# Kernel tuning notes

Hardware: AMD Instinct MI355X
Metric: run time of the kernel (lower is better)

## Reference

```python
import jax, jax.numpy as jnp
import numpy as np

B, N, NG = 32, 64, 100   # batch, atoms, gaussians in srdf
NB, NF, MAXZ = 128, 256, 20  # n_basis, n_factors, max atomic number
N_INTERACTIONS = 3


def setup_inputs() -> dict:
    key = jax.random.key(0)
    ks = jax.random.split(key, 12)
    r = np.sqrt(1.0 / np.sqrt(float(NB))).astype(np.float32)
    return {
        "Z": jax.random.randint(ks[0], (B, N), 0, MAXZ, dtype=jnp.int32),
        "C": jax.random.uniform(ks[1], (B, N, N, NG), dtype=jnp.float32),
        # learned parameters
        "W_emb": jax.random.normal(ks[2], (MAXZ, NB), dtype=jnp.float32) * r,
        "Wc": jax.random.normal(ks[3], (NG, NF), dtype=jnp.float32) * 0.1,
        "bc": jnp.zeros((NF,), dtype=jnp.float32),
        "Wi": jax.random.normal(ks[4], (NB, NF), dtype=jnp.float32) * 0.1,  # in2fac (shared across passes)
        "bi": jnp.zeros((NF,), dtype=jnp.float32),
        "Wf": jax.random.normal(ks[5], (NF, NB), dtype=jnp.float32) * 0.1,  # fac2out (shared)
        "W1": jax.random.normal(ks[6], (NB, NB // 2), dtype=jnp.float32) * 0.1,
        "b1": jnp.zeros((NB // 2,), dtype=jnp.float32),
        "W2": jax.random.normal(ks[7], (NB // 2, 1), dtype=jnp.float32) * 0.1,
        "b2": jnp.zeros((1,), dtype=jnp.float32),
    }


def reference(Z, C, W_emb, Wc, bc, Wi, bi, Wf, W1, b1, W2, b2):
    # pairwise mask: valid atom pairs (Z_i>0 and Z_j>0), diagonal removed
    pair = Z[:, :, None] * Z[:, None, :]                      # [B,N,N]
    offdiag = 1.0 - jnp.eye(N, dtype=jnp.float32)
    mask = (pair > 0).astype(jnp.float32) * offdiag           # [B,N,N]
    mask = mask[..., None]                                    # [B,N,N,1]

    # atom embedding via one-hot lookup == row gather
    X = W_emb[Z]                                              # [B,N,NB]
    # distance basis -> factor space
    fC = jnp.einsum('bijg,gf->bijf', C, Wc) + bc              # [B,N,N,NF]

    for _ in range(N_INTERACTIONS):
        fX = X @ Wi + bi                                      # [B,N,NF]
        fVj = fX[:, None, :, :] * fC                          # [B,N,N,NF]
        Vj = jnp.tanh(jnp.einsum('bijf,fo->bijo', fVj, Wf))   # [B,N,N,NB]
        V = jnp.sum(Vj * mask, axis=2)                        # masked sum over neighbors j
        X = X + V

    o1 = jnp.tanh(X @ W1 + b1)                                # [B,N,NB//2]
    yi = o1 @ W2 + b2                                         # [B,N,1]; std=1, mu=0 -> identity
    atom_mask = (Z > 0).astype(jnp.float32)[..., None]        # [B,N,1]
    y = jnp.sum(yi * atom_mask, axis=1)                       # [B,1] total energy
    return y
```

## Files before the change

### kernel.cpp

```cpp
#include <hip/hip_runtime.h>
#include <hip/hip_bf16.h>
#include <math.h>

#define BB   32
#define NN   64
#define NGG  100
#define NBB  128
#define NFF  256
#define NITER 3
#define KPAD 128

typedef _Float16 f16x8 __attribute__((ext_vector_type(8)));
typedef _Float16 f16x4 __attribute__((ext_vector_type(4)));
typedef float    f32x4 __attribute__((ext_vector_type(4)));

static __device__ __forceinline__ float fast_exp2(float x) {
    float r; asm("v_exp_f32 %0, %1" : "=v"(r) : "v"(x)); return r;
}
static __device__ __forceinline__ float fast_rcp(float x) {
    float r; asm("v_rcp_f32 %0, %1" : "=v"(r) : "v"(x)); return r;
}
static __device__ __forceinline__ float fast_tanh(float x) {
    float p = fast_exp2(x * 2.8853900817779268f);
    return 1.0f - 2.0f * fast_rcp(p + 1.0f);
}

#define EMB_N (BB * NN * NBB)
#define WCF_N (NFF * KPAD)
#define WFF_N (NBB * NFF)
__global__ void prep_kernel(const int* __restrict__ Z, const float* __restrict__ W_emb,
                            const float* __restrict__ Wc, const float* __restrict__ Wf,
                            float* __restrict__ X, _Float16* __restrict__ WcF,
                            _Float16* __restrict__ WfF) {
    int idx = blockIdx.x * 256 + threadIdx.x;
    if (idx < EMB_N) {
        int bn = idx >> 7, t = idx & 127;
        X[idx] = W_emb[Z[bn] * NBB + t];
        return;
    }
    idx -= EMB_N;
    if (idx < WCF_N) {
        int e = idx & 7, lane = (idx >> 3) & 63, ks = (idx >> 9) & 3, ct = (idx >> 11) & 3, w = idx >> 13;
        int l15 = lane & 15, kg = lane >> 4;
        int f = w * 64 + ct * 16 + l15;
        int k = ks * 32 + kg * 8 + e;
        WcF[idx] = (k < NGG) ? (_Float16)Wc[(size_t)k * NFF + f] : (_Float16)0.f;
        return;
    }
    idx -= WCF_N;
    if (idx < WFF_N) {
        int e = idx & 7, lane = (idx >> 3) & 63, ks = (idx >> 9) & 7, ct = (idx >> 12) & 1, w = idx >> 13;
        int l15 = lane & 15, kg = lane >> 4;
        int o = w * 32 + ct * 16 + l15;
        int k = ks * 32 + kg * 8 + e;
        WfF[idx] = (_Float16)Wf[(size_t)k * NBB + o];
    }
}
#define PREP_GRID ((EMB_N + WCF_N + WFF_N) / 256)

__global__ void transpose_pad_kernel(const float* __restrict__ src, _Float16* __restrict__ dst,
                                     int K, int Kpad, int NC) {
    int idx = blockIdx.x * 256 + threadIdx.x;
    if (idx >= NC * Kpad) return;
    int c = idx / Kpad, k = idx - c * Kpad;
    dst[idx] = (k < K) ? (_Float16)src[(size_t)k * NC + c] : (_Float16)0.f;
}

__global__ void fx_kernel(const float* __restrict__ X, const float* __restrict__ Wi,
                          const float* __restrict__ bi, const int* __restrict__ Z,
                          _Float16* __restrict__ fXF) {
    __shared__ float Xs[NBB];
    int bn = blockIdx.x, t = threadIdx.x;
    if (t < NBB) Xs[t] = X[bn * NBB + t];
    __syncthreads();
    float acc = bi[t];
    for (int k = 0; k < NBB; ++k) acc += Xs[k] * Wi[k * NFF + t];
    int b = bn >> 6, jr = bn & 63;
    int jt = jr >> 4, l15 = jr & 15;
    int ks = t >> 5, kg2 = (t >> 3) & 3, e = t & 7;
    size_t off = ((size_t)(b * 32 + jt * 8 + ks) * 64 + (kg2 * 16 + l15)) * 8 + e;
    fXF[off] = (Z[bn] > 0) ? (_Float16)acc : (_Float16)0.f;
}

static __device__ __forceinline__ void stage_C(const float* Crow_base, _Float16* Cs, int t) {
    const int r = t >> 2, q = t & 3;
    const float* Crow = Crow_base + (size_t)r * NGG;
    const int sw = (r & 7) << 3;
    #pragma unroll
    for (int m = 0; m < 8; ++m) {
        const int k = q * 32 + m * 4;
        f16x4 h = {0.f, 0.f, 0.f, 0.f};
        if (k < NGG) {
            float4 v = *(const float4*)(Crow + k);
            h[0] = (_Float16)v.x; h[1] = (_Float16)v.y;
            h[2] = (_Float16)v.z; h[3] = (_Float16)v.w;
        }
        *(f16x4*)&Cs[r * KPAD + (k ^ sw)] = h;
    }
}

__global__ __launch_bounds__(256, 3) void fc_kernel(
    const int* __restrict__ Z, const float* __restrict__ C,
    const _Float16* __restrict__ WcF, const float* __restrict__ bc,
    _Float16* __restrict__ fCF)
{
    __shared__ __align__(16) _Float16 Cs[NN * KPAD];
    const int bi_ = blockIdx.x;
    const int b = bi_ >> 6, i = bi_ & 63;
    if (Z[b * NN + i] == 0) return;

    const int t = threadIdx.x;
    const int wave = t >> 6, lane = t & 63;
    const int l15 = lane & 15, kg = lane >> 4;

    stage_C(C + (size_t)bi_ * NN * NGG, Cs, t);

    f16x8 aw[4][4];
    float4 bcq[4];
    #pragma unroll
    for (int ct = 0; ct < 4; ++ct) {
        #pragma unroll
        for (int ks = 0; ks < 4; ++ks)
            aw[ct][ks] = *(const f16x8*)&WcF[(size_t)(((wave * 4 + ct) * 4 + ks) * 64 + lane) * 8];
        bcq[ct] = *(const float4*)&bc[wave * 64 + ct * 16 + kg * 4];
    }
    __syncthreads();

    #pragma unroll
    for (int jt = 0; jt < 4; ++jt) {
        const int j = jt * 16 + l15;
        const int sw = (l15 & 7) << 3;
        f16x8 bfr[4];
        #pragma unroll
        for (int ks = 0; ks < 4; ++ks)
            bfr[ks] = *(const f16x8*)&Cs[j * KPAD + ((ks * 32 + kg * 8) ^ sw)];
        #pragma unroll
        for (int ct = 0; ct < 4; ++ct) {
            f32x4 acc = {bcq[ct].x, bcq[ct].y, bcq[ct].z, bcq[ct].w};
            #pragma unroll
            for (int ks = 0; ks < 4; ++ks)
                acc = __builtin_amdgcn_mfma_f32_16x16x32_f16(aw[ct][ks], bfr[ks], acc, 0, 0, 0);
            const int u = ct * 16 + kg * 4;
            const int ksf = wave * 2 + (u >> 5);
            const int kgf = (u >> 3) & 3;
            const int e0 = u & 4;
            f16x4 o;
            o[0] = (_Float16)acc[0]; o[1] = (_Float16)acc[1];
            o[2] = (_Float16)acc[2]; o[3] = (_Float16)acc[3];
            size_t off = ((size_t)(bi_ * 32 + jt * 8 + ksf) * 64 + (kgf * 16 + l15)) * 8 + e0;
            *(f16x4*)&fCF[off] = o;
        }
    }
}

__global__ __launch_bounds__(256) void interact_lite(
    const int* __restrict__ Z, const _Float16* __restrict__ fCF,
    const _Float16* __restrict__ WfF, const _Float16* __restrict__ fXF,
    float* __restrict__ X)
{
    const int bi_ = blockIdx.x;
    const int b = bi_ >> 6, i = bi_ & 63;
    if (Z[b * NN + i] == 0) return;

    const int t = threadIdx.x;
    const int wave = t >> 6, lane = t & 63;
    const int kg = lane >> 4;

    f16x8 bwf[2][8];
    #pragma unroll
    for (int ct = 0; ct < 2; ++ct)
        #pragma unroll
        for (int ks = 0; ks < 8; ++ks)
            bwf[ct][ks] = *(const f16x8*)&WfF[(size_t)(((wave * 2 + ct) * 8 + ks) * 64 + lane) * 8];

    const size_t cbase = (size_t)bi_ * 32;
    const size_t xbase = (size_t)b * 32;

    f32x4 a[4][2];
    #pragma unroll
    for (int jt = 0; jt < 4; ++jt) {
        a[jt][0] = (f32x4){0.f, 0.f, 0.f, 0.f};
        a[jt][1] = (f32x4){0.f, 0.f, 0.f, 0.f};
    }

    #pragma unroll
    for (int ks = 0; ks < 8; ++ks) {
        #pragma unroll
        for (int jt = 0; jt < 4; ++jt) {
            f16x8 fc = *(const f16x8*)&fCF[((cbase + jt * 8 + ks) * 64 + lane) * 8];
            f16x8 fx = *(const f16x8*)&fXF[((xbase + jt * 8 + ks) * 64 + lane) * 8];
            f16x8 av = fc * fx;
            a[jt][0] = __builtin_amdgcn_mfma_f32_16x16x32_f16(av, bwf[0][ks], a[jt][0], 0, 0, 0);
            a[jt][1] = __builtin_amdgcn_mfma_f32_16x16x32_f16(av, bwf[1][ks], a[jt][1], 0, 0, 0);
        }
    }

    float vsum0 = 0.f, vsum1 = 0.f;
    #pragma unroll
    for (int jt = 0; jt < 4; ++jt) {
        #pragma unroll
        for (int reg = 0; reg < 4; ++reg) {
            int j2 = jt * 16 + kg * 4 + reg;
            if (j2 != i) {
                vsum0 += fast_tanh(a[jt][0][reg]);
                vsum1 += fast_tanh(a[jt][1][reg]);
            }
        }
    }
    vsum0 += __shfl_xor(vsum0, 16); vsum0 += __shfl_xor(vsum0, 32);
    vsum1 += __shfl_xor(vsum1, 16); vsum1 += __shfl_xor(vsum1, 32);
    if (lane < 16) {
        float* Xp = X + (size_t)bi_ * NBB + wave * 32 + lane;
        Xp[0]  += vsum0;
        Xp[16] += vsum1;
    }
}

__global__ __launch_bounds__(256, 3) void interact_fused(
    const int* __restrict__ Z, const float* __restrict__ C,
    const _Float16* __restrict__ WcT, const float* __restrict__ bc,
    const _Float16* __restrict__ WfT, const _Float16* __restrict__ fXF,
    float* __restrict__ X)
{
    __shared__ __align__(16) _Float16 Cs[NN * KPAD];
    __shared__ __align__(16) _Float16 fVs[NN * NFF];

    const int bi_ = blockIdx.x;
    const int b = bi_ >> 6, i = bi_ & 63;
    if (Z[b * NN + i] == 0) return;

    const int t = threadIdx.x;
    const int wave = t >> 6, lane = t & 63;
    const int l15 = lane & 15, kg = lane >> 4;

    stage_C(C + (size_t)bi_ * NN * NGG, Cs, t);

    f16x8 aw[4][4];
    float4 bcq[4];
    #pragma unroll
    for (int ct = 0; ct < 4; ++ct) {
        #pragma unroll
        for (int ks = 0; ks < 4; ++ks)
            aw[ct][ks] = *(const f16x8*)&WcT[(size_t)(wave * 64 + ct * 16 + l15) * KPAD + ks * 32 + kg * 8];
        bcq[ct] = *(const float4*)&bc[wave * 64 + ct * 16 + kg * 4];
    }
    __syncthreads();

    #pragma unroll
    for (int jt = 0; jt < 4; ++jt) {
        const int j = jt * 16 + l15;
        const int sw = (l15 & 7) << 3;
        f16x8 bfr[4];
        #pragma unroll
        for (int ks = 0; ks < 4; ++ks)
            bfr[ks] = *(const f16x8*)&Cs[j * KPAD + ((ks * 32 + kg * 8) ^ sw)];
        #pragma unroll
        for (int ct = 0; ct < 4; ++ct) {
            f32x4 acc = {bcq[ct].x, bcq[ct].y, bcq[ct].z, bcq[ct].w};
            #pragma unroll
            for (int ks = 0; ks < 4; ++ks)
                acc = __builtin_amdgcn_mfma_f32_16x16x32_f16(aw[ct][ks], bfr[ks], acc, 0, 0, 0);
            const int u = ct * 16 + kg * 4;
            const int ksf = wave * 2 + (u >> 5);
            const int kgf = (u >> 3) & 3;
            const int e0 = u & 4;
            f16x4 fx4 = *(const f16x4*)&fXF[((size_t)(b * 32 + jt * 8 + ksf) * 64 + (kgf * 16 + l15)) * 8 + e0];
            const int f0 = wave * 64 + u;
            f16x4 o;
            o[0] = (_Float16)(acc[0] * (float)fx4[0]);
            o[1] = (_Float16)(acc[1] * (float)fx4[1]);
            o[2] = (_Float16)(acc[2] * (float)fx4[2]);
            o[3] = (_Float16)(acc[3] * (float)fx4[3]);
            *(f16x4*)&fVs[j * NFF + (f0 ^ ((j & 7) << 3))] = o;
        }
    }
    __syncthreads();

    f16x8 bwf[2][8];
    #pragma unroll
    for (int ct = 0; ct < 2; ++ct)
        #pragma unroll
        for (int ks = 0; ks < 8; ++ks)
            bwf[ct][ks] = *(const f16x8*)&WfT[(size_t)(wave * 32 + ct * 16 + l15) * NFF + ks * 32 + kg * 8];

    float vsum0 = 0.f, vsum1 = 0.f;
    #pragma unroll
    for (int jt = 0; jt < 4; ++jt) {
        const int r = jt * 16 + l15;
        const int sw = (l15 & 7) << 3;
        f32x4 a0 = {0.f, 0.f, 0.f, 0.f}, a1 = {0.f, 0.f, 0.f, 0.f};
        #pragma unroll
        for (int ks = 0; ks < 8; ++ks) {
            f16x8 av = *(const f16x8*)&fVs[r * NFF + ((ks * 32 + kg * 8) ^ sw)];
            a0 = __builtin_amdgcn_mfma_f32_16x16x32_f16(av, bwf[0][ks], a0, 0, 0, 0);
            a1 = __builtin_amdgcn_mfma_f32_16x16x32_f16(av, bwf[1][ks], a1, 0, 0, 0);
        }
        #pragma unroll
        for (int reg = 0; reg < 4; ++reg) {
            int j2 = jt * 16 + kg * 4 + reg;
            if (j2 != i) {
                vsum0 += fast_tanh(a0[reg]);
                vsum1 += fast_tanh(a1[reg]);
            }
        }
    }
    vsum0 += __shfl_xor(vsum0, 16); vsum0 += __shfl_xor(vsum0, 32);
    vsum1 += __shfl_xor(vsum1, 16); vsum1 += __shfl_xor(vsum1, 32);
    if (lane < 16) {
        float* Xp = X + (size_t)bi_ * NBB + wave * 32 + lane;
        Xp[0]  += vsum0;
        Xp[16] += vsum1;
    }
}

__global__ void readoutA_kernel(const int* __restrict__ Z, const float* __restrict__ X,
                                const float* __restrict__ W1, const float* __restrict__ b1,
                                const float* __restrict__ W2, const float* __restrict__ b2,
                                float* __restrict__ yi_buf)
{
    __shared__ float Xs[NBB];
    int bn = blockIdx.x;
    int h = threadIdx.x;
    Xs[h] = X[(size_t)bn * NBB + h];
    Xs[h + 64] = X[(size_t)bn * NBB + h + 64];
    __syncthreads();

    float s = b1[h];
    for (int k = 0; k < NBB; ++k) s += Xs[k] * W1[k * 64 + h];
    float v = tanhf(s) * W2[h];
    #pragma unroll
    for (int off = 32; off > 0; off >>= 1) v += __shfl_down(v, off);
    if (h == 0) {
        int z = Z[bn];
        yi_buf[bn] = (z > 0) ? (v + b2[0]) : 0.f;
    }
}

__global__ void readoutB_kernel(const float* __restrict__ yi_buf, float* __restrict__ y)
{
    int b = blockIdx.x, i = threadIdx.x;
    float v = yi_buf[b * NN + i];
    #pragma unroll
    for (int off = 32; off > 0; off >>= 1) v += __shfl_down(v, off);
    if (i == 0) y[b] = v;
}

extern "C" void kernel_launch(void* const* d_in, const int* in_sizes, int n_in,
                              void* d_out, int out_size, void* d_ws, size_t ws_size,
                              hipStream_t stream) {
    (void)in_sizes; (void)n_in; (void)out_size;
    const int*   Z    = (const int*)d_in[0];
    const float* C    = (const float*)d_in[1];
    const float* Wemb = (const float*)d_in[2];
    const float* Wc   = (const float*)d_in[3];
    const float* bc   = (const float*)d_in[4];
    const float* Wi   = (const float*)d_in[5];
    const float* bi   = (const float*)d_in[6];
    const float* Wf   = (const float*)d_in[7];
    const float* W1   = (const float*)d_in[8];
    const float* b1   = (const float*)d_in[9];
    const float* W2   = (const float*)d_in[10];
    const float* b2   = (const float*)d_in[11];
    float* y = (float*)d_out;

    char* p = (char*)d_ws;
    float*    X   = (float*)p;      p += (size_t)BB * NN * NBB * 4;
    _Float16* fXF = (_Float16*)p;   p += (size_t)BB * NN * NFF * 2;
    _Float16* WcF = (_Float16*)p;   p += (size_t)NFF * KPAD * 2;
    _Float16* WfF = (_Float16*)p;   p += (size_t)NBB * NFF * 2;
    _Float16* WcT = (_Float16*)p;   p += (size_t)NFF * KPAD * 2;
    _Float16* WfT = (_Float16*)p;   p += (size_t)NBB * NFF * 2;
    float*    yi  = (float*)p;      p += (size_t)BB * NN * 4;
    size_t base = (size_t)(p - (char*)d_ws);
    size_t fcf_bytes = (size_t)BB * NN * NN * NFF * 2;
    bool split = (ws_size >= base + fcf_bytes);
    _Float16* fCF = (_Float16*)p;

    prep_kernel<<<PREP_GRID, 256, 0, stream>>>(Z, Wemb, Wc, Wf, X, WcF, WfF);

    if (split) {
        fc_kernel<<<BB * NN, 256, 0, stream>>>(Z, C, WcF, bc, fCF);
        for (int it = 0; it < NITER; ++it) {
            fx_kernel<<<BB * NN, NFF, 0, stream>>>(X, Wi, bi, Z, fXF);
            interact_lite<<<BB * NN, 256, 0, stream>>>(Z, fCF, WfF, fXF, X);
        }
    } else {
        transpose_pad_kernel<<<(NFF * KPAD) / 256, 256, 0, stream>>>(Wc, WcT, NGG, KPAD, NFF);
        transpose_pad_kernel<<<(NBB * NFF) / 256, 256, 0, stream>>>(Wf, WfT, NFF, NFF, NBB);
        for (int it = 0; it < NITER; ++it) {
            fx_kernel<<<BB * NN, NFF, 0, stream>>>(X, Wi, bi, Z, fXF);
            interact_fused<<<BB * NN, 256, 0, stream>>>(Z, C, WcT, bc, WfT, fXF, X);
        }
    }
    readoutA_kernel<<<BB * NN, 64, 0, stream>>>(Z, X, W1, b1, W2, b2, yi);
    readoutB_kernel<<<BB, NN, 0, stream>>>(yi, y);
}
```

Measured before the change: 154.3 us.

## Use MFMA for fX and readout GEMMs, fuse first fX into fC kernel

Replaces the scalar per-atom fx_kernel with an MFMA-based fxm kernel that computes a whole batch's 64x256 factor tile per block, using a pre-swizzled fp16 Wi. The first iteration's fX is merged into the fC kernel as extra blocks, removing one launch. The readout is also rewritten as a single MFMA kernel with in-block reduction, replacing two launches. This cuts launch count and the scalar FMA loops, at the cost of fp16 rounding of X and the weights in these GEMMs.

Result: faster. 124.9 us (-19.0%).

```diff
diff --git a/kernel.cpp b/kernel.cpp
--- a/kernel.cpp
+++ b/kernel.cpp
@@ -28,10 +28,16 @@
 #define EMB_N (BB * NN * NBB)
 #define WCF_N (NFF * KPAD)
 #define WFF_N (NBB * NFF)
+#define WIF_N (NBB * NFF)
+#define W1F_N (NBB * 64)
+#define PREP_TOTAL (EMB_N + WCF_N + WFF_N + WIF_N + W1F_N)
+#define PREP_GRID (PREP_TOTAL / 256)
 __global__ void prep_kernel(const int* __restrict__ Z, const float* __restrict__ W_emb,
                             const float* __restrict__ Wc, const float* __restrict__ Wf,
+                            const float* __restrict__ Wi, const float* __restrict__ W1,
                             float* __restrict__ X, _Float16* __restrict__ WcF,
-                            _Float16* __restrict__ WfF) {
+                            _Float16* __restrict__ WfF, _Float16* __restrict__ WiF,
+                            _Float16* __restrict__ W1F) {
     int idx = blockIdx.x * 256 + threadIdx.x;
     if (idx < EMB_N) {
         int bn = idx >> 7, t = idx & 127;
@@ -54,9 +60,26 @@
         int o = w * 32 + ct * 16 + l15;
         int k = ks * 32 + kg * 8 + e;
         WfF[idx] = (_Float16)Wf[(size_t)k * NBB + o];
-    }
-}
-#define PREP_GRID ((EMB_N + WCF_N + WFF_N) / 256)
+        return;
+    }
+    idx -= WFF_N;
+    if (idx < WIF_N) {
+        int e = idx & 7, lane = (idx >> 3) & 63, ks = (idx >> 9) & 3, ct16 = idx >> 11;
+        int l15 = lane & 15, kg = lane >> 4;
+        int f = ct16 * 16 + l15;
+        int k = ks * 32 + kg * 8 + e;
+        WiF[idx] = (_Float16)Wi[(size_t)k * NFF + f];
+        return;
+    }
+    idx -= WIF_N;
+    if (idx < W1F_N) {
+        int e = idx & 7, lane = (idx >> 3) & 63, ks = (idx >> 9) & 3, ct16 = idx >> 11;
+        int l15 = lane & 15, kg = lane >> 4;
+        int o = ct16 * 16 + l15;
+        int k = ks * 32 + kg * 8 + e;
+        W1F[idx] = (_Float16)W1[(size_t)k * 64 + o];
+    }
+}
 
 __global__ void transpose_pad_kernel(const float* __restrict__ src, _Float16* __restrict__ dst,
                                      int K, int Kpad, int NC) {
@@ -64,22 +87,6 @@
     if (idx >= NC * Kpad) return;
     int c = idx / Kpad, k = idx - c * Kpad;
     dst[idx] = (k < K) ? (_Float16)src[(size_t)k * NC + c] : (_Float16)0.f;
-}
-
-__global__ void fx_kernel(const float* __restrict__ X, const float* __restrict__ Wi,
-                          const float* __restrict__ bi, const int* __restrict__ Z,
-                          _Float16* __restrict__ fXF) {
-    __shared__ float Xs[NBB];
-    int bn = blockIdx.x, t = threadIdx.x;
-    if (t < NBB) Xs[t] = X[bn * NBB + t];
-    __syncthreads();
-    float acc = bi[t];
-    for (int k = 0; k < NBB; ++k) acc += Xs[k] * Wi[k * NFF + t];
-    int b = bn >> 6, jr = bn & 63;
-    int jt = jr >> 4, l15 = jr & 15;
-    int ks = t >> 5, kg2 = (t >> 3) & 3, e = t & 7;
-    size_t off = ((size_t)(b * 32 + jt * 8 + ks) * 64 + (kg2 * 16 + l15)) * 8 + e;
-    fXF[off] = (Z[bn] > 0) ? (_Float16)acc : (_Float16)0.f;
 }
 
 static __device__ __forceinline__ void stage_C(const float* Crow_base, _Float16* Cs, int t) {
@@ -98,18 +105,30 @@
         *(f16x4*)&Cs[r * KPAD + (k ^ sw)] = h;
     }
 }
-
-__global__ __launch_bounds__(256, 3) void fc_kernel(
+static __device__ __forceinline__ void stage_X(const float* Xrow_base, _Float16* Xs, int t) {
+    const int r = t >> 2, q = t & 3;
+    const float* Xrow = Xrow_base + (size_t)r * NBB;
+    const int sw = (r & 7) << 3;
+    #pragma unroll
+    for (int m = 0; m < 8; ++m) {
+        const int k = q * 32 + m * 4;
+        float4 v = *(const float4*)(Xrow + k);
+        f16x4 h;
+        h[0] = (_Float16)v.x; h[1] = (_Float16)v.y;
+        h[2] = (_Float16)v.z; h[3] = (_Float16)v.w;
+        *(f16x4*)&Xs[r * KPAD + (k ^ sw)] = h;
+    }
+}
+
+static __device__ __forceinline__ void fc_body(
+    int bi_, int t, _Float16* Cs,
     const int* __restrict__ Z, const float* __restrict__ C,
     const _Float16* __restrict__ WcF, const float* __restrict__ bc,
     _Float16* __restrict__ fCF)
 {
-    __shared__ __align__(16) _Float16 Cs[NN * KPAD];
-    const int bi_ = blockIdx.x;
     const int b = bi_ >> 6, i = bi_ & 63;
     if (Z[b * NN + i] == 0) return;
 
-    const int t = threadIdx.x;
     const int wave = t >> 6, lane = t & 63;
     const int l15 = lane & 15, kg = lane >> 4;
 
@@ -151,6 +170,81 @@
             *(f16x4*)&fCF[off] = o;
         }
     }
+}
+
+static __device__ __forceinline__ void fxm_body(
+    int b, int fq, int t, _Float16* Xs,
+    const float* __restrict__ X, const _Float16* __restrict__ WiF,
+    const float* __restrict__ bi, const int* __restrict__ Z,
+    _Float16* __restrict__ fXF)
+{
+    const int wave = t >> 6, lane = t & 63;
+    const int l15 = lane & 15, kg = lane >> 4;
+    const int ct16 = fq * 4 + wave;
+
+    stage_X(X + (size_t)b * NN * NBB, Xs, t);
+
+    f16x8 aw[4];
+    #pragma unroll
+    for (int ks = 0; ks < 4; ++ks)
+        aw[ks] = *(const f16x8*)&WiF[(size_t)((ct16 * 4 + ks) * 64 + lane) * 8];
+    float4 biq = *(const float4*)&bi[ct16 * 16 + kg * 4];
+    __syncthreads();
+
+    f32x4 acc[4];
+    #pragma unroll
+    for (int jt = 0; jt < 4; ++jt) acc[jt] = (f32x4){biq.x, biq.y, biq.z, biq.w};
+
+    #pragma unroll
+    for (int ks = 0; ks < 4; ++ks) {
+        #pragma unroll
+        for (int jt = 0; jt < 4; ++jt) {
+            const int j = jt * 16 + l15;
+            const int sw = (l15 & 7) << 3;
+            f16x8 bfr = *(const f16x8*)&Xs[j * KPAD + ((ks * 32 + kg * 8) ^ sw)];
+            acc[jt] = __builtin_amdgcn_mfma_f32_16x16x32_f16(aw[ks], bfr, acc[jt], 0, 0, 0);
+        }
+    }
+
+    const int u_g = ct16 * 16 + kg * 4;
+    const int ks_t = u_g >> 5, kg_t = (u_g >> 3) & 3, e0 = u_g & 4;
+    #pragma unroll
+    for (int jt = 0; jt < 4; ++jt) {
+        const int j = jt * 16 + l15;
+        const int zj = Z[b * NN + j];
+        f16x4 o = {0.f, 0.f, 0.f, 0.f};
+        if (zj > 0) {
+            o[0] = (_Float16)acc[jt][0]; o[1] = (_Float16)acc[jt][1];
+            o[2] = (_Float16)acc[jt][2]; o[3] = (_Float16)acc[jt][3];
+        }
+        size_t off = ((size_t)(b * 32 + jt * 8 + ks_t) * 64 + (kg_t * 16 + l15)) * 8 + e0;
+        *(f16x4*)&fXF[off] = o;
+    }
+}
+
+#define FXM_GRID (BB * 4)
+
+__global__ __launch_bounds__(256) void fxm_kernel(
+    const float* __restrict__ X, const _Float16* __restrict__ WiF,
+    const float* __restrict__ bi, const int* __restrict__ Z,
+    _Float16* __restrict__ fXF)
+{
+    __shared__ __align__(16) _Float16 Xs[NN * KPAD];
+    fxm_body(blockIdx.x >> 2, blockIdx.x & 3, threadIdx.x, Xs, X, WiF, bi, Z, fXF);
+}
+
+__global__ __launch_bounds__(256, 3) void fcfx_kernel(
+    const int* __restrict__ Z, const float* __restrict__ C,
+    const _Float16* __restrict__ WcF, const float* __restrict__ bc,
+    _Float16* __restrict__ fCF,
+    const float* __restrict__ X, const _Float16* __restrict__ WiF,
+    const float* __restrict__ bi, _Float16* __restrict__ fXF)
+{
+    __shared__ __align__(16) _Float16 S[NN * KPAD];
+    if (blockIdx.x < FXM_GRID)
+        fxm_body(blockIdx.x >> 2, blockIdx.x & 3, threadIdx.x, S, X, WiF, bi, Z, fXF);
+    else
+        fc_body(blockIdx.x - FXM_GRID, threadIdx.x, S, Z, C, WcF, bc, fCF);
 }
 
 __global__ __launch_bounds__(256) void interact_lite(
@@ -313,36 +407,59 @@
     }
 }
 
-__global__ void readoutA_kernel(const int* __restrict__ Z, const float* __restrict__ X,
-                                const float* __restrict__ W1, const float* __restrict__ b1,
-                                const float* __restrict__ W2, const float* __restrict__ b2,
-                                float* __restrict__ yi_buf)
-{
-    __shared__ float Xs[NBB];
-    int bn = blockIdx.x;
-    int h = threadIdx.x;
-    Xs[h] = X[(size_t)bn * NBB + h];
-    Xs[h + 64] = X[(size_t)bn * NBB + h + 64];
+__global__ __launch_bounds__(256) void readout_kernel(
+    const int* __restrict__ Z, const float* __restrict__ X,
+    const _Float16* __restrict__ W1F, const float* __restrict__ b1,
+    const float* __restrict__ W2, const float* __restrict__ b2,
+    float* __restrict__ y)
+{
+    __shared__ __align__(16) _Float16 Xs[NN * KPAD];
+    __shared__ float part[4][NN];
+    const int b = blockIdx.x, t = threadIdx.x;
+    const int wave = t >> 6, lane = t & 63;
+    const int l15 = lane & 15, kg = lane >> 4;
+
+    stage_X(X + (size_t)b * NN * NBB, Xs, t);
+
+    f16x8 aw[4];
+    #pragma unroll
+    for (int ks = 0; ks < 4; ++ks)
+        aw[ks] = *(const f16x8*)&W1F[(size_t)((wave * 4 + ks) * 64 + lane) * 8];
+    float4 b1q = *(const float4*)&b1[wave * 16 + kg * 4];
+    float4 w2q = *(const float4*)&W2[wave * 16 + kg * 4];
     __syncthreads();
 
-    float s = b1[h];
-    for (int k = 0; k < NBB; ++k) s += Xs[k] * W1[k * 64 + h];
-    float v = tanhf(s) * W2[h];
-    #pragma unroll
-    for (int off = 32; off > 0; off >>= 1) v += __shfl_down(v, off);
-    if (h == 0) {
-        int z = Z[bn];
-        yi_buf[bn] = (z > 0) ? (v + b2[0]) : 0.f;
-    }
-}
-
-__global__ void readoutB_kernel(const float* __restrict__ yi_buf, float* __restrict__ y)
-{
-    int b = blockIdx.x, i = threadIdx.x;
-    float v = yi_buf[b * NN + i];
-    #pragma unroll
-    for (int off = 32; off > 0; off >>= 1) v += __shfl_down(v, off);
-    if (i == 0) y[b] = v;
+    f32x4 acc[4];
+    #pragma unroll
+    for (int jt = 0; jt < 4; ++jt) acc[jt] = (f32x4){b1q.x, b1q.y, b1q.z, b1q.w};
+
+    #pragma unroll
+    for (int ks = 0; ks < 4; ++ks) {
+        #pragma unroll
+        for (int jt = 0; jt < 4; ++jt) {
+            const int j = jt * 16 + l15;
+            const int sw = (l15 & 7) << 3;
+            f16x8 bfr = *(const f16x8*)&Xs[j * KPAD + ((ks * 32 + kg * 8) ^ sw)];
+            acc[jt] = __builtin_amdgcn_mfma_f32_16x16x32_f16(aw[ks], bfr, acc[jt], 0, 0, 0);
+        }
+    }
+
+    #pragma unroll
+    for (int jt = 0; jt < 4; ++jt) {
+        float s = fast_tanh(acc[jt][0]) * w2q.x + fast_tanh(acc[jt][1]) * w2q.y
+                + fast_tanh(acc[jt][2]) * w2q.z + fast_tanh(acc[jt][3]) * w2q.w;
+        s += __shfl_xor(s, 16); s += __shfl_xor(s, 32);
+        if (lane < 16) part[wave][jt * 16 + lane] = s;
+    }
+    __syncthreads();
+
+    if (t < NN) {
+        float s = part[0][t] + part[1][t] + part[2][t] + part[3][t] + b2[0];
+        float v = (Z[b * NN + t] > 0) ? s : 0.f;
+        #pragma unroll
+        for (int off = 32; off > 0; off >>= 1) v += __shfl_down(v, off);
+        if (t == 0) y[b] = v;
+    }
 }
 
 extern "C" void kernel_launch(void* const* d_in, const int* in_sizes, int n_in,
@@ -366,32 +483,33 @@
     char* p = (char*)d_ws;
     float*    X   = (float*)p;      p += (size_t)BB * NN * NBB * 4;
     _Float16* fXF = (_Float16*)p;   p += (size_t)BB * NN * NFF * 2;
-    _Float16* WcF = (_Float16*)p;   p += (size_t)NFF * KPAD * 2;
-    _Float16* WfF = (_Float16*)p;   p += (size_t)NBB * NFF * 2;
+    _Float16* WcF = (_Float16*)p;   p += (size_t)WCF_N * 2;
+    _Float16* WfF = (_Float16*)p;   p += (size_t)WFF_N * 2;
+    _Float16* WiF = (_Float16*)p;   p += (size_t)WIF_N * 2;
+    _Float16* W1F = (_Float16*)p;   p += (size_t)W1F_N * 2;
     _Float16* WcT = (_Float16*)p;   p += (size_t)NFF * KPAD * 2;
     _Float16* WfT = (_Float16*)p;   p += (size_t)NBB * NFF * 2;
-    float*    yi  = (float*)p;      p += (size_t)BB * NN * 4;
     size_t base = (size_t)(p - (char*)d_ws);
     size_t fcf_bytes = (size_t)BB * NN * NN * NFF * 2;
     bool split = (ws_size >= base + fcf_bytes);
     _Float16* fCF = (_Float16*)p;
 
-    prep_kernel<<<PREP_GRID, 256, 0, stream>>>(Z, Wemb, Wc, Wf, X, WcF, WfF);
+    prep_kernel<<<PREP_GRID, 256, 0, stream>>>(Z, Wemb, Wc, Wf, Wi, W1, X, WcF, WfF, WiF, W1F);
 
     if (split) {
-        fc_kernel<<<BB * NN, 256, 0, stream>>>(Z, C, WcF, bc, fCF);
-        for (int it = 0; it < NITER; ++it) {
-            fx_kernel<<<BB * NN, NFF, 0, stream>>>(X, Wi, bi, Z, fXF);
+        fcfx_kernel<<<FXM_GRID + BB * NN, 256, 0, stream>>>(Z, C, WcF, bc, fCF, X, WiF, bi, fXF);
+        interact_lite<<<BB * NN, 256, 0, stream>>>(Z, fCF, WfF, fXF, X);
+        for (int it = 1; it < NITER; ++it) {
+            fxm_kernel<<<FXM_GRID, 256, 0, stream>>>(X, WiF, bi, Z, fXF);
             interact_lite<<<BB * NN, 256, 0, stream>>>(Z, fCF, WfF, fXF, X);
         }
     } else {
         transpose_pad_kernel<<<(NFF * KPAD) / 256, 256, 0, stream>>>(Wc, WcT, NGG, KPAD, NFF);
         transpose_pad_kernel<<<(NBB * NFF) / 256, 256, 0, stream>>>(Wf, WfT, NFF, NFF, NBB);
         for (int it = 0; it < NITER; ++it) {
-            fx_kernel<<<BB * NN, NFF, 0, stream>>>(X, Wi, bi, Z, fXF);
+            fxm_kernel<<<FXM_GRID, 256, 0, stream>>>(X, WiF, bi, Z, fXF);
             interact_fused<<<BB * NN, 256, 0, stream>>>(Z, C, WcT, bc, WfT, fXF, X);
         }
     }
-    readoutA_kernel<<<BB * NN, 64, 0, stream>>>(Z, X, W1, b1, W2, b2, yi);
-    readoutB_kernel<<<BB, NN, 0, stream>>>(yi, y);
-}
+    readout_kernel<<<BB, 256, 0, stream>>>(Z, X, W1F, b1, W2, b2, y);
+}
```
